# Performance work log

Hardware: AMD Instinct MI355X
Metric: run time of the kernel (lower is better)

Reference implementation:

```python
import jax, jax.numpy as jnp
import numpy as np

B, N, D = 8192, 512, 3

def setup_inputs() -> dict:
    key = jax.random.key(0)
    k1, k2 = jax.random.split(key)
    inp = jax.random.normal(k1, (B, N, D), dtype=jnp.float32)
    tgt = jax.random.normal(k2, (B, N, D), dtype=jnp.float32)
    return {"input": inp, "target": tgt}

def _kabsch_rotation(x, y):
    # x, y: (B, N, 3) centered. Covariance C: (B, 3, 3)
    C = jnp.einsum('bji,bjk->bik', x, y)
    U, _, Vh = jnp.linalg.svd(C, full_matrices=False)
    d = jnp.linalg.det(U) * jnp.linalg.det(Vh)  # (B,)
    # flip sign of last row of Vh where det is negative (proper rotation)
    Vh = Vh.at[:, -1, :].multiply(d[:, None])
    return U @ Vh  # (B, 3, 3)

def reference(input, target):
    x = input - input.mean(-2, keepdims=True)
    y = target - target.mean(-2, keepdims=True)
    R = _kabsch_rotation(x, y)
    aligned = jnp.einsum('bnd,bde->bne', x, R)
    return jnp.mean((aligned - y) ** 2)
```

## Files before the change

### kernel.cpp

```cpp
#include <hip/hip_runtime.h>
#include <math.h>

#define B_TOT 8192
#define N_PTS 512
#define WAVES_PER_BLOCK 4
#define BLK_A (64 * WAVES_PER_BLOCK)

__device__ __forceinline__ float dpp_wave_sum(float v) {
    int x;
    x = __builtin_amdgcn_update_dpp(0, __float_as_int(v), 0x111, 0xF, 0xF, true);
    v += __int_as_float(x);
    x = __builtin_amdgcn_update_dpp(0, __float_as_int(v), 0x112, 0xF, 0xF, true);
    v += __int_as_float(x);
    x = __builtin_amdgcn_update_dpp(0, __float_as_int(v), 0x114, 0xF, 0xF, true);
    v += __int_as_float(x);
    x = __builtin_amdgcn_update_dpp(0, __float_as_int(v), 0x118, 0xF, 0xF, true);
    v += __int_as_float(x);
    x = __builtin_amdgcn_update_dpp(0, __float_as_int(v), 0x142, 0xF, 0xF, true);
    v += __int_as_float(x);
    x = __builtin_amdgcn_update_dpp(0, __float_as_int(v), 0x143, 0xF, 0xF, true);
    v += __int_as_float(x);
    return v;
}

__global__ __launch_bounds__(BLK_A) void sums_kernel(const float* __restrict__ x,
                                                     const float* __restrict__ y,
                                                     float* __restrict__ ws)
{
    const int wave = threadIdx.x >> 6;
    const int lane = threadIdx.x & 63;
    const int b = blockIdx.x * WAVES_PER_BLOCK + wave;

    const float4* xb = reinterpret_cast<const float4*>(x) + (size_t)b * 384 + 6 * lane;
    const float4* yb = reinterpret_cast<const float4*>(y) + (size_t)b * 384 + 6 * lane;

    union { float4 v[6]; float f[24]; } X, Y;
    #pragma unroll
    for (int i = 0; i < 6; i++) { X.v[i] = xb[i]; Y.v[i] = yb[i]; }

    float acc[17];
    #pragma unroll
    for (int k = 0; k < 17; k++) acc[k] = 0.f;

    #pragma unroll
    for (int p = 0; p < 8; p++) {
        float x0 = X.f[3*p], x1 = X.f[3*p+1], x2 = X.f[3*p+2];
        float y0 = Y.f[3*p], y1 = Y.f[3*p+1], y2 = Y.f[3*p+2];
        acc[0] += x0;  acc[1] += x1;  acc[2] += x2;
        acc[3] += y0;  acc[4] += y1;  acc[5] += y2;
        acc[6]  += x0*y0; acc[7]  += x0*y1; acc[8]  += x0*y2;
        acc[9]  += x1*y0; acc[10] += x1*y1; acc[11] += x1*y2;
        acc[12] += x2*y0; acc[13] += x2*y1; acc[14] += x2*y2;
        acc[15] += x0*x0 + x1*x1 + x2*x2;
        acc[16] += y0*y0 + y1*y1 + y2*y2;
    }

    #pragma unroll
    for (int k = 0; k < 17; k++) acc[k] = dpp_wave_sum(acc[k]);

    if (lane == 63) {
        #pragma unroll
        for (int k = 0; k < 17; k++) ws[k * B_TOT + b] = acc[k];
    }
}

__global__ __launch_bounds__(256) void solve_kernel(const float* __restrict__ ws,
                                                    double* __restrict__ blockSums)
{
    const int b = blockIdx.x * 256 + threadIdx.x;

    double S[17];
    #pragma unroll
    for (int k = 0; k < 17; k++) S[k] = (double)ws[k * B_TOT + b];

    const double Nn = (double)N_PTS;
    double mx[3] = {S[0]/Nn, S[1]/Nn, S[2]/Nn};
    double my[3] = {S[3]/Nn, S[4]/Nn, S[5]/Nn};

    double C[3][3];
    #pragma unroll
    for (int d = 0; d < 3; d++)
        #pragma unroll
        for (int e = 0; e < 3; e++)
            C[d][e] = S[6 + d*3 + e] - Nn * mx[d] * my[e];

    double sxx = S[15] - Nn*(mx[0]*mx[0] + mx[1]*mx[1] + mx[2]*mx[2]);
    double syy = S[16] - Nn*(my[0]*my[0] + my[1]*my[1] + my[2]*my[2]);

    double K00=0,K01=0,K02=0,K11=0,K12=0,K22=0;
    #pragma unroll
    for (int k = 0; k < 3; k++) {
        K00 += C[k][0]*C[k][0]; K01 += C[k][0]*C[k][1]; K02 += C[k][0]*C[k][2];
        K11 += C[k][1]*C[k][1]; K12 += C[k][1]*C[k][2]; K22 += C[k][2]*C[k][2];
    }

    double q3 = (K00 + K11 + K22) / 3.0;
    double p1 = K01*K01 + K02*K02 + K12*K12;
    double a00 = K00 - q3, a11 = K11 - q3, a22 = K22 - q3;
    double p2 = a00*a00 + a11*a11 + a22*a22 + 2.0*p1;
    double lam1, lam2, lam3;
    if (p2 <= 1e-300) {
        lam1 = lam2 = lam3 = q3;
    } else {
        double pp  = sqrt(p2 / 6.0);
        double ip  = 1.0 / pp;
        double b00 = a00*ip, b11 = a11*ip, b22 = a22*ip;
        double b01 = K01*ip, b02 = K02*ip, b12 = K12*ip;
        double detB = b00*(b11*b22 - b12*b12)
                    - b01*(b01*b22 - b12*b02)
                    + b02*(b01*b12 - b11*b02);
        double r = 0.5 * detB;
        r = fmin(1.0, fmax(-1.0, r));
        double phi = acos(r) / 3.0;
        lam1 = q3 + 2.0*pp*cos(phi);
        lam3 = q3 + 2.0*pp*cos(phi + 2.0943951023931954923);
        lam2 = 3.0*q3 - lam1 - lam3;
    }
    lam1 = fmax(lam1, 0.0); lam2 = fmax(lam2, 0.0); lam3 = fmax(lam3, 0.0);
    double s1 = sqrt(lam1), s2 = sqrt(lam2), s3 = sqrt(lam3);

    double detC = C[0][0]*(C[1][1]*C[2][2] - C[1][2]*C[2][1])
                - C[0][1]*(C[1][0]*C[2][2] - C[1][2]*C[2][0])
                + C[0][2]*(C[1][0]*C[2][1] - C[1][1]*C[2][0]);
    double sgn = (detC < 0.0) ? -1.0 : 1.0;
    double trRC = s1 + s2 + sgn * s3;

    double v = sxx + syy - 2.0 * trRC;

    #pragma unroll
    for (int off = 32; off; off >>= 1) v += __shfl_down(v, off, 64);
    __shared__ double red[4];
    const int wave = threadIdx.x >> 6, lane = threadIdx.x & 63;
    if (lane == 0) red[wave] = v;
    __syncthreads();
    if (threadIdx.x == 0)
        blockSums[blockIdx.x] = red[0] + red[1] + red[2] + red[3];
}

__global__ __launch_bounds__(64) void final_kernel(const double* __restrict__ bs,
                                                   float* __restrict__ out)
{
    const int t = threadIdx.x;
    double v = (t < 32) ? bs[t] : 0.0;
    #pragma unroll
    for (int off = 32; off; off >>= 1) v += __shfl_down(v, off, 64);
    if (t == 0)
        out[0] = (float)(v / ((double)B_TOT * (double)N_PTS * 3.0));
}

extern "C" void kernel_launch(void* const* d_in, const int* in_sizes, int n_in,
                              void* d_out, int out_size, void* d_ws, size_t ws_size,
                              hipStream_t stream) {
    const float* x = (const float*)d_in[0];
    const float* y = (const float*)d_in[1];
    float* out = (float*)d_out;

    float*  ws = (float*)d_ws;
    double* bs = (double*)((char*)d_ws + 17 * B_TOT * 4);

    sums_kernel <<<B_TOT / WAVES_PER_BLOCK, BLK_A, 0, stream>>>(x, y, ws);
    solve_kernel<<<B_TOT / 256, 256, 0, stream>>>(ws, bs);
    final_kernel<<<1, 64, 0, stream>>>(bs, out);
}
```

Measured before the change: 121.6 us.

## Fuse final reduction into solve via atomics and switch to coalesced per-point loads

Removes the third kernel launch by having each solve block atomically add its partial sum and letting the last block, found through an atomic counter, write the final mean. The accumulator and counter are reset at the start of the sums kernel. The load pattern also changes from six contiguous float4 loads per lane to strided 12-byte struct loads in which consecutive lanes read consecutive points. This aims to cut launch overhead, but the double-precision atomic adds make the summation order nondeterministic, and the 12-byte loads may be less efficient than float4 loads.

```diff
diff --git a/kernel.cpp b/kernel.cpp
--- a/kernel.cpp
+++ b/kernel.cpp
@@ -5,6 +5,8 @@
 #define N_PTS 512
 #define WAVES_PER_BLOCK 4
 #define BLK_A (64 * WAVES_PER_BLOCK)
+
+struct f3 { float x, y, z; };
 
 __device__ __forceinline__ float dpp_wave_sum(float v) {
     int x;
@@ -25,47 +27,49 @@
 
 __global__ __launch_bounds__(BLK_A) void sums_kernel(const float* __restrict__ x,
                                                      const float* __restrict__ y,
-                                                     float* __restrict__ ws)
+                                                     float* __restrict__ ws,
+                                                     double* __restrict__ acc_out,
+                                                     unsigned* __restrict__ cnt)
 {
+    if (blockIdx.x == 0 && threadIdx.x == 0) { *acc_out = 0.0; *cnt = 0u; }
+
     const int wave = threadIdx.x >> 6;
     const int lane = threadIdx.x & 63;
     const int b = blockIdx.x * WAVES_PER_BLOCK + wave;
 
-    const float4* xb = reinterpret_cast<const float4*>(x) + (size_t)b * 384 + 6 * lane;
-    const float4* yb = reinterpret_cast<const float4*>(y) + (size_t)b * 384 + 6 * lane;
+    const f3* __restrict__ xb = reinterpret_cast<const f3*>(x) + (size_t)b * N_PTS;
+    const f3* __restrict__ yb = reinterpret_cast<const f3*>(y) + (size_t)b * N_PTS;
 
-    union { float4 v[6]; float f[24]; } X, Y;
+    float a[17];
     #pragma unroll
-    for (int i = 0; i < 6; i++) { X.v[i] = xb[i]; Y.v[i] = yb[i]; }
-
-    float acc[17];
-    #pragma unroll
-    for (int k = 0; k < 17; k++) acc[k] = 0.f;
+    for (int k = 0; k < 17; k++) a[k] = 0.f;
 
     #pragma unroll
     for (int p = 0; p < 8; p++) {
-        float x0 = X.f[3*p], x1 = X.f[3*p+1], x2 = X.f[3*p+2];
-        float y0 = Y.f[3*p], y1 = Y.f[3*p+1], y2 = Y.f[3*p+2];
-        acc[0] += x0;  acc[1] += x1;  acc[2] += x2;
-        acc[3] += y0;  acc[4] += y1;  acc[5] += y2;
-        acc[6]  += x0*y0; acc[7]  += x0*y1; acc[8]  += x0*y2;
-        acc[9]  += x1*y0; acc[10] += x1*y1; acc[11] += x1*y2;
-        acc[12] += x2*y0; acc[13] += x2*y1; acc[14] += x2*y2;
-        acc[15] += x0*x0 + x1*x1 + x2*x2;
-        acc[16] += y0*y0 + y1*y1 + y2*y2;
+        f3 X = xb[p * 64 + lane];
+        f3 Y = yb[p * 64 + lane];
+        a[0] += X.x;  a[1] += X.y;  a[2] += X.z;
+        a[3] += Y.x;  a[4] += Y.y;  a[5] += Y.z;
+        a[6]  += X.x*Y.x; a[7]  += X.x*Y.y; a[8]  += X.x*Y.z;
+        a[9]  += X.y*Y.x; a[10] += X.y*Y.y; a[11] += X.y*Y.z;
+        a[12] += X.z*Y.x; a[13] += X.z*Y.y; a[14] += X.z*Y.z;
+        a[15] += X.x*X.x + X.y*X.y + X.z*X.z;
+        a[16] += Y.x*Y.x + Y.y*Y.y + Y.z*Y.z;
     }
 
     #pragma unroll
-    for (int k = 0; k < 17; k++) acc[k] = dpp_wave_sum(acc[k]);
+    for (int k = 0; k < 17; k++) a[k] = dpp_wave_sum(a[k]);
 
     if (lane == 63) {
         #pragma unroll
-        for (int k = 0; k < 17; k++) ws[k * B_TOT + b] = acc[k];
+        for (int k = 0; k < 17; k++) ws[k * B_TOT + b] = a[k];
     }
 }
 
 __global__ __launch_bounds__(256) void solve_kernel(const float* __restrict__ ws,
-                                                    double* __restrict__ blockSums)
+                                                    double* __restrict__ acc_out,
+                                                    unsigned* __restrict__ cnt,
+                                                    float* __restrict__ out)
 {
     const int b = blockIdx.x * 256 + threadIdx.x;
 
@@ -133,19 +137,18 @@
     const int wave = threadIdx.x >> 6, lane = threadIdx.x & 63;
     if (lane == 0) red[wave] = v;
     __syncthreads();
-    if (threadIdx.x == 0)
-        blockSums[blockIdx.x] = red[0] + red[1] + red[2] + red[3];
-}
 
-__global__ __launch_bounds__(64) void final_kernel(const double* __restrict__ bs,
-                                                   float* __restrict__ out)
-{
-    const int t = threadIdx.x;
-    double v = (t < 32) ? bs[t] : 0.0;
-    #pragma unroll
-    for (int off = 32; off; off >>= 1) v += __shfl_down(v, off, 64);
-    if (t == 0)
-        out[0] = (float)(v / ((double)B_TOT * (double)N_PTS * 3.0));
+    if (threadIdx.x == 0) {
+        double blk = red[0] + red[1] + red[2] + red[3];
+        atomicAdd(acc_out, blk);
+        __threadfence();
+        unsigned t = atomicAdd(cnt, 1u);
+        if (t == gridDim.x - 1) {
+            __threadfence();
+            double total = atomicAdd(acc_out, 0.0);
+            out[0] = (float)(total / ((double)B_TOT * (double)N_PTS * 3.0));
+        }
+    }
 }
 
 extern "C" void kernel_launch(void* const* d_in, const int* in_sizes, int n_in,
@@ -155,10 +158,10 @@
     const float* y = (const float*)d_in[1];
     float* out = (float*)d_out;
 
-    float*  ws = (float*)d_ws;
-    double* bs = (double*)((char*)d_ws + 17 * B_TOT * 4);
+    float*    ws  = (float*)d_ws;
+    double*   acc = (double*)((char*)d_ws + 17 * B_TOT * 4);
+    unsigned* cnt = (unsigned*)((char*)d_ws + 17 * B_TOT * 4 + 8);
 
-    sums_kernel <<<B_TOT / WAVES_PER_BLOCK, BLK_A, 0, stream>>>(x, y, ws);
-    solve_kernel<<<B_TOT / 256, 256, 0, stream>>>(ws, bs);
-    final_kernel<<<1, 64, 0, stream>>>(bs, out);
+    sums_kernel <<<B_TOT / WAVES_PER_BLOCK, BLK_A, 0, stream>>>(x, y, ws, acc, cnt);
+    solve_kernel<<<B_TOT / 256, 256, 0, stream>>>(ws, acc, cnt, out);
 }
```

After: 116.7 us, median of 2. 1.04x faster.
